# Kernel tuning notes

Hardware: AMD Instinct MI355X
Metric: run time of the kernel (lower is better)

## Reference

```python
import jax, jax.numpy as jnp
import numpy as np

N = 40000
E = 200000
D = 32
NUM_BANDS = 3
ORDER = 4
EPS = 1e-8
LN_EPS = 1e-5


def setup_inputs() -> dict:
    key = jax.random.key(0)
    ks = jax.random.split(key, 20)
    h = jax.random.normal(ks[0], (N, D), dtype=jnp.float32)
    Q = jax.random.normal(ks[1], (E, D, D), dtype=jnp.float32) / jnp.sqrt(jnp.float32(D))
    edge_index = jax.random.randint(ks[2], (2, E), 0, N, dtype=jnp.int32)
    coeffs = jnp.ones((NUM_BANDS, ORDER + 1), dtype=jnp.float32) / (ORDER + 1)
    s = 1.0 / np.sqrt(D)
    proj_W = jax.random.uniform(ks[3], (NUM_BANDS, D, D), minval=-s, maxval=s, dtype=jnp.float32)
    proj_b = jax.random.uniform(ks[4], (NUM_BANDS, D), minval=-s, maxval=s, dtype=jnp.float32)
    proj_g = jnp.ones((NUM_BANDS, D), dtype=jnp.float32)
    proj_beta = jnp.zeros((NUM_BANDS, D), dtype=jnp.float32)
    s3 = 1.0 / np.sqrt(NUM_BANDS * D)
    fus_W1 = jax.random.uniform(ks[5], (NUM_BANDS * D, D), minval=-s3, maxval=s3, dtype=jnp.float32)
    fus_b1 = jax.random.uniform(ks[6], (D,), minval=-s3, maxval=s3, dtype=jnp.float32)
    fus_g = jnp.ones((D,), dtype=jnp.float32)
    fus_beta = jnp.zeros((D,), dtype=jnp.float32)
    fus_W2 = jax.random.uniform(ks[7], (D, D), minval=-s, maxval=s, dtype=jnp.float32)
    fus_b2 = jax.random.uniform(ks[8], (D,), minval=-s, maxval=s, dtype=jnp.float32)
    return {"h": h, "Q": Q, "edge_index": edge_index, "coeffs": coeffs,
            "proj_W": proj_W, "proj_b": proj_b, "proj_g": proj_g, "proj_beta": proj_beta,
            "fus_W1": fus_W1, "fus_b1": fus_b1, "fus_g": fus_g, "fus_beta": fus_beta,
            "fus_W2": fus_W2, "fus_b2": fus_b2}


def _layer_norm(x, g, b):
    mu = x.mean(-1, keepdims=True)
    var = x.var(-1, keepdims=True)  # biased, as torch LayerNorm
    return (x - mu) / jnp.sqrt(var + LN_EPS) * g + b


def reference(h, Q, edge_index, coeffs, proj_W, proj_b, proj_g, proj_beta,
              fus_W1, fus_b1, fus_g, fus_beta, fus_W2, fus_b2):
    row, col = edge_index[0], edge_index[1]
    n = h.shape[0]
    ones_e = jnp.ones(row.shape[0], dtype=h.dtype)
    deg = (jax.ops.segment_sum(ones_e, row, num_segments=n)
           + jax.ops.segment_sum(ones_e, col, num_segments=n))  # [N]

    def matvec(x):
        # gather -> per-edge DxD bmm -> scatter_add; diag via degree
        Qh = jnp.einsum('eij,ej->ei', Q, x[col])          # [E, D]
        off = jax.ops.segment_sum(Qh, row, num_segments=n)  # [N, D]
        return deg[:, None] * x - off

    # power iteration for lambda_max (5 iters, fixed key for determinism)
    v = jax.random.normal(jax.random.key(42), h.shape, dtype=h.dtype)
    v = v / jnp.linalg.norm(v)
    lam = jnp.array(1.0, dtype=h.dtype)
    for _ in range(5):
        Lv = matvec(v)
        lam = (v * Lv).sum() / ((v * v).sum() + EPS)
        v = Lv / (jnp.linalg.norm(Lv) + EPS)
    lam = jnp.maximum(lam, 1.0)

    def L_tilde(x):
        return 2.0 / (lam + EPS) * matvec(x) - x

    bands = []
    for b_idx in range(NUM_BANDS):
        w = jax.nn.softmax(coeffs[b_idx])
        T_prev = h
        T_curr = L_tilde(h)
        res = w[0] * T_prev + w[1] * T_curr
        for k in range(2, ORDER + 1):
            T_next = 2.0 * L_tilde(T_curr) - T_prev
            res = res + w[k] * T_next
            T_prev, T_curr = T_curr, T_next
        p = jax.nn.silu(_layer_norm(res @ proj_W[b_idx] + proj_b[b_idx],
                                    proj_g[b_idx], proj_beta[b_idx]))
        bands.append(p)

    cat = jnp.concatenate(bands, axis=-1)  # [N, 3D]
    fused = jax.nn.silu(_layer_norm(cat @ fus_W1 + fus_b1, fus_g, fus_beta)) @ fus_W2 + fus_b2
    return h + fused
```

## Files before the change

kernel.cpp:

```cpp
#include <hip/hip_runtime.h>
#include <hip/hip_fp16.h>
#include <math.h>

#define NN 40000
#define EE 200000
#define DD 32
#define ND (NN * DD)
#define LNEPS 1e-5f

typedef float    fv4 __attribute__((ext_vector_type(4)));
typedef unsigned uv4 __attribute__((ext_vector_type(4)));

#define SLOT_ALPHA 48
#define SCAL_FLOATS (64 + 2048 + 64)

__device__ __forceinline__ void threefry2x32(unsigned k0, unsigned k1,
                                             unsigned x0, unsigned x1,
                                             unsigned& o0, unsigned& o1) {
  const unsigned k2 = k0 ^ k1 ^ 0x1BD11BDAu;
  unsigned v0 = x0 + k0, v1 = x1 + k1;
#define TF_ROUND(r) { v0 += v1; v1 = (v1 << (r)) | (v1 >> (32 - (r))); v1 ^= v0; }
  TF_ROUND(13) TF_ROUND(15) TF_ROUND(26) TF_ROUND(6)
  v0 += k1; v1 += k2 + 1u;
  TF_ROUND(17) TF_ROUND(29) TF_ROUND(16) TF_ROUND(24)
  v0 += k2; v1 += k0 + 2u;
  TF_ROUND(13) TF_ROUND(15) TF_ROUND(26) TF_ROUND(6)
  v0 += k0; v1 += k1 + 3u;
  TF_ROUND(17) TF_ROUND(29) TF_ROUND(16) TF_ROUND(24)
  v0 += k1; v1 += k2 + 4u;
  TF_ROUND(13) TF_ROUND(15) TF_ROUND(26) TF_ROUND(6)
  v0 += k2; v1 += k0 + 5u;
#undef TF_ROUND
  o0 = v0; o1 = v1;
}

__device__ __forceinline__ float wave64_sum(float x) {
  for (int o = 32; o > 0; o >>= 1) x += __shfl_xor(x, o, 64);
  return x;
}
__device__ __forceinline__ float g32_sum(float x) {
  for (int o = 16; o > 0; o >>= 1) x += __shfl_xor(x, o, 32);
  return x;
}

__global__ void k_deg(const int* __restrict__ ei, float* __restrict__ deg,
                      int* __restrict__ hist) {
  int e = blockIdx.x * 256 + threadIdx.x;
  if (e < EE) {
    int r = ei[e];
    atomicAdd(deg + r, 1.0f);
    atomicAdd(deg + ei[EE + e], 1.0f);
    atomicAdd(hist + r, 1);
  }
}

__global__ __launch_bounds__(1024) void k_scan(const int* __restrict__ hist,
                                               int* __restrict__ row_start,
                                               int* __restrict__ cursor) {
  __shared__ int part[1024];
  const int t = threadIdx.x;
  const int base = t * 40;
  int s = 0;
  for (int i = base; i < base + 40 && i < NN; ++i) s += hist[i];
  part[t] = s;
  __syncthreads();
  for (int off = 1; off < 1024; off <<= 1) {
    int v = (t >= off) ? part[t - off] : 0;
    __syncthreads();
    part[t] += v;
    __syncthreads();
  }
  int ex = (t == 0) ? 0 : part[t - 1];
  for (int i = base; i < base + 40 && i < NN; ++i) {
    row_start[i] = ex;
    cursor[i] = ex;
    ex += hist[i];
  }
  if (t == 0) row_start[NN] = EE;
}

__global__ void k_genv(float* __restrict__ v, float* __restrict__ vpre,
                       const float* __restrict__ deg) {
  int i = blockIdx.x * 256 + threadIdx.x;
  unsigned o0, o1;
  threefry2x32(0u, 42u, 0u, (unsigned)i, o0, o1);
  unsigned bits = o1;
  float f = __uint_as_float((bits >> 9) | 0x3f800000u) - 1.0f;
  const float lo = -0.99999994f;
  float u = fmaxf(lo, f * 2.0f + lo);
  float val = 1.41421354f * erfinvf(u);
  v[i] = val;
  if (vpre) vpre[i] = deg[i >> 5] * val;
}

__device__ __forceinline__ int clamp8(float q) {
  int v = (int)rintf(q);
  return v < -127 ? -127 : (v > 127 ? 127 : v);
}
__device__ __forceinline__ unsigned pack4v(fv4 q, float inv) {
  int q0 = clamp8(q.x * inv), q1 = clamp8(q.y * inv),
      q2 = clamp8(q.z * inv), q3 = clamp8(q.w * inv);
  return (q0 & 255) | ((q1 & 255) << 8) | ((q2 & 255) << 16) | ((q3 & 255) << 24);
}
__device__ __forceinline__ void dp4(unsigned u, fv4 xv, float& acc) {
  acc = fmaf((float)(signed char)(u),        xv.x, acc);
  acc = fmaf((float)(signed char)(u >> 8),   xv.y, acc);
  acc = fmaf((float)(signed char)(u >> 16),  xv.z, acc);
  acc = fmaf((float)(signed char)(u >> 24),  xv.w, acc);
}

__global__ __launch_bounds__(256) void k_cvt_mv(const float* __restrict__ x,
                                                const float* __restrict__ Q,
                                                const int* __restrict__ ei,
                                                int* __restrict__ cursor,
                                                char* __restrict__ Qi8,
                                                __half* __restrict__ Qs,
                                                int* __restrict__ cols,
                                                float* __restrict__ out) {
  const int slot = threadIdx.x >> 5;
  const int lane = threadIdx.x & 31;
  const int e = blockIdx.x * 8 + slot;
  const int row = ei[e];
  const int col = ei[EE + e];
  int pos = 0;
  if (lane == 0) pos = atomicAdd(cursor + row, 1);
  pos = __shfl(pos, 0, 32);
  const fv4* __restrict__ x4 = (const fv4*)(x + (size_t)col * DD);
  fv4 xr[8];
#pragma unroll
  for (int k = 0; k < 8; ++k) xr[k] = x4[k];
  const fv4* __restrict__ q4 =
      (const fv4*)(Q + (size_t)e * (DD * DD) + (size_t)lane * DD);
  fv4 qf[8];
#pragma unroll
  for (int k = 0; k < 8; ++k) qf[k] = __builtin_nontemporal_load(q4 + k);
  float acc = 0.0f;
#pragma unroll
  for (int k = 0; k < 8; ++k) {
    acc = fmaf(qf[k].x, xr[k].x, acc);
    acc = fmaf(qf[k].y, xr[k].y, acc);
    acc = fmaf(qf[k].z, xr[k].z, acc);
    acc = fmaf(qf[k].w, xr[k].w, acc);
  }
  float m = 0.0f;
#pragma unroll
  for (int k = 0; k < 8; ++k) {
    m = fmaxf(m, fmaxf(fmaxf(fabsf(qf[k].x), fabsf(qf[k].y)),
                       fmaxf(fabsf(qf[k].z), fabsf(qf[k].w))));
  }
  __half sh = __float2half(m * (1.0f / 127.0f));
  float s = __half2float(sh);
  float inv = (s > 0.0f) ? 1.0f / s : 0.0f;
  uv4 pa, pb;
  pa.x = pack4v(qf[0], inv); pa.y = pack4v(qf[1], inv);
  pa.z = pack4v(qf[2], inv); pa.w = pack4v(qf[3], inv);
  pb.x = pack4v(qf[4], inv); pb.y = pack4v(qf[5], inv);
  pb.z = pack4v(qf[6], inv); pb.w = pack4v(qf[7], inv);
  uv4* __restrict__ qs = (uv4*)(Qi8 + (size_t)pos * (DD * DD) + (size_t)lane * DD);
  qs[0] = pa;
  qs[1] = pb;
  Qs[pos * DD + lane] = sh;
  if (lane == 0) cols[pos] = col;
  atomicAdd(out + (size_t)row * DD + lane, -acc);
}

#define CHUNK 16

__global__ __launch_bounds__(256) void k_gather2(const float* __restrict__ px,
                                                 float* __restrict__ pout,
                                                 const float* __restrict__ kxv,
                                                 float* __restrict__ kout,
                                                 const char* __restrict__ Qi8,
                                                 const __half* __restrict__ Qs,
                                                 const int* __restrict__ cols,
                                                 const int* __restrict__ row_start,
                                                 const float* __restrict__ deg,
                                                 float* __restrict__ dots,
                                                 int do_dots) {
  __shared__ float lds[4][CHUNK][DD];
  __shared__ float d1[4], d2[4];
  const int NB = NN / 4;
  const bool isk = blockIdx.x >= NB;
  const int bid = isk ? blockIdx.x - NB : blockIdx.x;
  const float* __restrict__ x = isk ? kxv : px;
  float* __restrict__ out = isk ? kout : pout;

  const int wid  = threadIdx.x >> 6;
  const int lane = threadIdx.x & 63;
  const int half = lane >> 5;
  const int d    = lane & 31;
  const int r = bid * 4 + wid;
  const int beg = row_start[r];
  const int end = row_start[r + 1];
  const int degree = end - beg;

  const size_t idx = (size_t)r * DD + d;
  const float xi = x[idx];
  const float dv = deg[r];

  float acc = 0.0f;
  for (int chunk = 0; chunk < degree; chunk += CHUNK) {
    const int nchunk = min(CHUNK, degree - chunk);
    int myc = (lane < nchunk) ? cols[beg + chunk + lane] : 0;
    {
      const int el = lane >> 2;
      const int pt = lane & 3;
      if (el < nchunk) {
        const int c = __shfl(myc, el, 64);
        const fv4* __restrict__ xs = (const fv4*)(x + (size_t)c * DD);
        fv4 a = xs[pt * 2];
        fv4 b = xs[pt * 2 + 1];
        fv4* __restrict__ dst = (fv4*)&lds[wid][el][pt * 8];
        dst[0] = a;
        dst[1] = b;
      }
    }
    uv4 a0 = {0,0,0,0}, b0 = {0,0,0,0}, a1 = {0,0,0,0}, b1 = {0,0,0,0};
    float s0 = 0.0f, s1 = 0.0f;
#define LOADQ(PP, A, B, S)                                                    \
    if ((PP) < nchunk) {                                                      \
      const size_t pos = (size_t)(beg + chunk + (PP));                        \
      const uv4* __restrict__ q8 =                                            \
          (const uv4*)(Qi8 + pos * (DD * DD) + (size_t)d * DD);               \
      A = q8[0]; B = q8[1];                                                   \
      S = __half2float(Qs[pos * DD + d]);                                     \
    }
    LOADQ(half, a0, b0, s0)
    LOADQ(2 + half, a1, b1, s1)
    for (int p0 = 0; p0 < nchunk; p0 += 2) {
      uv4 a2 = {0,0,0,0}, b2 = {0,0,0,0};
      float s2 = 0.0f;
      LOADQ(p0 + 4 + half, a2, b2, s2)
      const int p = p0 + half;
      if (p < nchunk) {
        const fv4* __restrict__ xl = (const fv4*)&lds[wid][p][0];
        fv4 xr[8];
#pragma unroll
        for (int k = 0; k < 8; ++k) xr[k] = xl[k];
        float dot = 0.0f;
        dp4(a0.x, xr[0], dot); dp4(a0.y, xr[1], dot);
        dp4(a0.z, xr[2], dot); dp4(a0.w, xr[3], dot);
        dp4(b0.x, xr[4], dot); dp4(b0.y, xr[5], dot);
        dp4(b0.z, xr[6], dot); dp4(b0.w, xr[7], dot);
        acc = fmaf(s0, dot, acc);
      }
      a0 = a1; b0 = b1; s0 = s1;
      a1 = a2; b1 = b2; s1 = s2;
    }
#undef LOADQ
  }
  acc += __shfl_xor(acc, 32, 64);

  const float o = dv * xi - acc;
  if (half == 0) out[idx] = o;

  if (!isk && do_dots) {
    float p1 = (half == 0) ? o * xi : 0.0f;
    float p2 = (half == 0) ? xi * xi : 0.0f;
    p1 = wave64_sum(p1);
    p2 = wave64_sum(p2);
    if ((threadIdx.x & 63) == 0) { d1[wid] = p1; d2[wid] = p2; }
    __syncthreads();
    if (threadIdx.x == 0) {
      const int leaf = bid & 31;
      atomicAdd(dots + 64 + leaf * 32, d1[0] + d1[1] + d1[2] + d1[3]);
      atomicAdd(dots + 64 + 1024 + leaf * 32, d2[0] + d2[1] + d2[2] + d2[3]);
    }
  }
}

__global__ void k_pre(const float* __restrict__ x, const float* __restrict__ deg,
                      float* __restrict__ out) {
  int i = blockIdx.x * 256 + threadIdx.x;
  out[i] = deg[i >> 5] * x[i];
}

__global__ __launch_bounds__(256) void k_matvec(const float* __restrict__ x,
                                                const float* __restrict__ Q,
                                                const int* __restrict__ ei,
                                                float* __restrict__ out) {
  const int slot = threadIdx.x >> 5;
  const int lane = threadIdx.x & 31;
  const int e = blockIdx.x * 8 + slot;
  const int row = ei[e];
  const int col = ei[EE + e];
  const fv4* __restrict__ x4 = (const fv4*)(x + (size_t)col * DD);
  fv4 xr[8];
#pragma unroll
  for (int k = 0; k < 8; ++k) xr[k] = x4[k];
  const fv4* __restrict__ q4 =
      (const fv4*)(Q + (size_t)e * (DD * DD) + (size_t)lane * DD);
  float acc = 0.0f;
#pragma unroll
  for (int k = 0; k < 8; ++k) {
    fv4 q = q4[k];
    acc = fmaf(q.x, xr[k].x, acc);
    acc = fmaf(q.y, xr[k].y, acc);
    acc = fmaf(q.z, xr[k].z, acc);
    acc = fmaf(q.w, xr[k].w, acc);
  }
  atomicAdd(out + (size_t)row * DD + lane, -acc);
}

#define DOT_BLOCKS 640
__global__ void k_dots(const float* __restrict__ u4, const float* __restrict__ u5,
                       float* __restrict__ scal) {
  float s1 = 0.0f, s2 = 0.0f;
  for (int i = blockIdx.x * 256 + threadIdx.x; i < ND; i += DOT_BLOCKS * 256) {
    float a = u4[i], b = u5[i];
    s1 = fmaf(a, b, s1);
    s2 = fmaf(a, a, s2);
  }
  s1 = wave64_sum(s1);
  s2 = wave64_sum(s2);
  __shared__ float ls1[4], ls2[4];
  int w = threadIdx.x >> 6;
  if ((threadIdx.x & 63) == 0) { ls1[w] = s1; ls2[w] = s2; }
  __syncthreads();
  if (threadIdx.x == 0) {
    atomicAdd(scal + 64, ls1[0] + ls1[1] + ls1[2] + ls1[3]);
    atomicAdd(scal + 64 + 1024, ls2[0] + ls2[1] + ls2[2] + ls2[3]);
  }
}

__global__ void k_alpha(float* __restrict__ scal) {
  float S1 = 0.0f, S2 = 0.0f;
  for (int l = 0; l < 32; ++l) {
    S1 += scal[64 + l * 32];
    S2 += scal[64 + 1024 + l * 32];
  }
  float lam = S1 / S2 / (1.0f + 1e-8f);
  lam = fmaxf(lam, 1.0f);
  scal[SLOT_ALPHA] = 2.0f / (lam + 1e-8f);
}

__global__ __launch_bounds__(256) void k_fuse(
    const float* __restrict__ h,
    const float* __restrict__ W1, const float* __restrict__ W2,
    const float* __restrict__ W3, const float* __restrict__ W4,
    const float* __restrict__ scal,
    const float* __restrict__ coeffs,
    const float* __restrict__ projW, const float* __restrict__ projb,
    const float* __restrict__ projg, const float* __restrict__ projbeta,
    const float* __restrict__ fusW1, const float* __restrict__ fusb1,
    const float* __restrict__ fusg, const float* __restrict__ fusbeta,
    const float* __restrict__ fusW2, const float* __restrict__ fusb2,
    float* __restrict__ out) {
  __shared__ float s_res[8][3][DD];
  __shared__ float s_p[8][3 * DD];
  __shared__ float s_s[8][DD];
  const int slot = threadIdx.x >> 5;
  const int lane = threadIdx.x & 31;
  const int n = blockIdx.x * 8 + slot;

  float w[3][5];
#pragma unroll
  for (int b = 0; b < 3; ++b) {
    float m = -1e30f;
#pragma unroll
    for (int k = 0; k < 5; ++k) m = fmaxf(m, coeffs[b * 5 + k]);
    float s = 0.0f;
#pragma unroll
    for (int k = 0; k < 5; ++k) { w[b][k] = expf(coeffs[b * 5 + k] - m); s += w[b][k]; }
#pragma unroll
    for (int k = 0; k < 5; ++k) w[b][k] /= s;
  }

  const float C[5][5] = {
      { 1.0f,   0.0f,   0.0f,   0.0f,  0.0f},
      {-1.0f,   1.0f,   0.0f,   0.0f,  0.0f},
      { 1.0f,  -4.0f,   2.0f,   0.0f,  0.0f},
      {-1.0f,   9.0f, -12.0f,   4.0f,  0.0f},
      { 1.0f, -16.0f,  40.0f, -32.0f,  8.0f}};
  float cb[3][5];
#pragma unroll
  for (int b = 0; b < 3; ++b)
#pragma unroll
    for (int j = 0; j < 5; ++j) {
      float c = 0.0f;
#pragma unroll
      for (int k = 0; k < 5; ++k) c = fmaf(w[b][k], C[k][j], c);
      cb[b][j] = c;
    }

  const float alpha = scal[SLOT_ALPHA];
  const float a1 = alpha, a2 = a1 * alpha, a3 = a2 * alpha, a4 = a3 * alpha;

  const int idx = n * DD + lane;
  const float hd = h[idx];
  float y[5];
  y[0] = hd;
  y[1] = a1 * W1[idx];
  y[2] = a2 * W2[idx];
  y[3] = a3 * W3[idx];
  y[4] = a4 * W4[idx];
#pragma unroll
  for (int b = 0; b < 3; ++b) {
    float res = 0.0f;
#pragma unroll
    for (int j = 0; j < 5; ++j) res = fmaf(cb[b][j], y[j], res);
    s_res[slot][b][lane] = res;
  }
  __syncthreads();

#pragma unroll
  for (int b = 0; b < 3; ++b) {
    float yv = projb[b * DD + lane];
#pragma unroll
    for (int j = 0; j < DD; ++j)
      yv = fmaf(s_res[slot][b][j], projW[(b * DD + j) * DD + lane], yv);
    float mu = g32_sum(yv) * (1.0f / DD);
    float dv = yv - mu;
    float var = g32_sum(dv * dv) * (1.0f / DD);
    float z = dv * rsqrtf(var + LNEPS) * projg[b * DD + lane] + projbeta[b * DD + lane];
    float pb = z / (1.0f + expf(-z));
    s_p[slot][b * DD + lane] = pb;
  }
  __syncthreads();

  float yv = fusb1[lane];
#pragma unroll
  for (int j = 0; j < 3 * DD; ++j)
    yv = fmaf(s_p[slot][j], fusW1[j * DD + lane], yv);
  float mu = g32_sum(yv) * (1.0f / DD);
  float dv = yv - mu;
  float var = g32_sum(dv * dv) * (1.0f / DD);
  float z = dv * rsqrtf(var + LNEPS) * fusg[lane] + fusbeta[lane];
  float sv = z / (1.0f + expf(-z));
  s_s[slot][lane] = sv;
  __syncthreads();

  float o = fusb2[lane];
#pragma unroll
  for (int j = 0; j < DD; ++j)
    o = fmaf(s_s[slot][j], fusW2[j * DD + lane], o);
  out[idx] = hd + o;
}

extern "C" void kernel_launch(void* const* d_in, const int* in_sizes, int n_in,
                              void* d_out, int out_size, void* d_ws, size_t ws_size,
                              hipStream_t stream) {
  (void)in_sizes; (void)n_in; (void)out_size;
  const float* h        = (const float*)d_in[0];
  const float* Q        = (const float*)d_in[1];
  const int*   ei       = (const int*)d_in[2];
  const float* coeffs   = (const float*)d_in[3];
  const float* projW    = (const float*)d_in[4];
  const float* projb    = (const float*)d_in[5];
  const float* projg    = (const float*)d_in[6];
  const float* projbeta = (const float*)d_in[7];
  const float* fusW1    = (const float*)d_in[8];
  const float* fusb1    = (const float*)d_in[9];
  const float* fusg     = (const float*)d_in[10];
  const float* fusbeta  = (const float*)d_in[11];
  const float* fusW2    = (const float*)d_in[12];
  const float* fusb2    = (const float*)d_in[13];
  float* out = (float*)d_out;

  const size_t qi_bytes  = (size_t)EE * DD * DD;
  const size_t qs_bytes  = (size_t)EE * DD * sizeof(__half);
  const size_t col_bytes = (size_t)EE * sizeof(int);
  const size_t idx_bytes = (size_t)(2 * NN + 2) * sizeof(int);
  const size_t f32_elems = 6u * (size_t)ND + 2u * NN + SCAL_FLOATS;
  const size_t meta = qi_bytes + qs_bytes + col_bytes + idx_bytes;
  const size_t need = meta + f32_elems * sizeof(float) + 512;
  const bool fast = ws_size >= need;

  char*   Qi8 = (char*)d_ws;
  __half* Qs  = (__half*)((char*)d_ws + qi_bytes);
  int*  cols      = (int*)((char*)d_ws + qi_bytes + qs_bytes);
  int*  row_start = cols + EE;
  int*  cursor    = row_start + NN + 1;
  float* base = fast
      ? (float*)((char*)d_ws + ((meta + 255) & ~(size_t)255))
      : (float*)d_ws;
  float* uA   = base;
  float* uB   = uA + ND;
  float* W1   = uB + ND;
  float* W2   = W1 + ND;
  float* W3   = W2 + ND;
  float* W4   = W3 + ND;
  float* deg  = W4 + ND;
  float* scal = deg + NN;
  int*   hist = (int*)(scal + SCAL_FLOATS);

  (void)hipMemsetAsync(deg, 0, (2 * (size_t)NN + SCAL_FLOATS) * sizeof(float),
                       stream);

  k_deg<<<(EE + 255) / 256, 256, 0, stream>>>(ei, deg, hist);

  if (fast) {
    k_genv<<<ND / 256, 256, 0, stream>>>(uA, uB, deg);
    k_scan<<<1, 1024, 0, stream>>>(hist, row_start, cursor);
    k_cvt_mv<<<EE / 8, 256, 0, stream>>>(uA, Q, ei, cursor, Qi8, Qs, cols, uB);

    const int G2 = 2 * (NN / 4);
    k_gather2<<<G2, 256, 0, stream>>>(uB, uA, h,  W1, Qi8, Qs, cols,
                                      row_start, deg, scal, 0);
    k_gather2<<<G2, 256, 0, stream>>>(uA, uB, W1, W2, Qi8, Qs, cols,
                                      row_start, deg, scal, 0);
    k_gather2<<<G2, 256, 0, stream>>>(uB, uA, W2, W3, Qi8, Qs, cols,
                                      row_start, deg, scal, 0);
    k_gather2<<<G2, 256, 0, stream>>>(uA, uB, W3, W4, Qi8, Qs, cols,
                                      row_start, deg, scal, 1);
    k_alpha<<<1, 1, 0, stream>>>(scal);
  } else {
    k_genv<<<ND / 256, 256, 0, stream>>>(uA, nullptr, deg);
    float* cur = uA;
    float* nxt = uB;
    for (int it = 0; it < 5; ++it) {
      k_pre<<<ND / 256, 256, 0, stream>>>(cur, deg, nxt);
      k_matvec<<<EE / 8, 256, 0, stream>>>(cur, Q, ei, nxt);
      float* t = cur; cur = nxt; nxt = t;
    }
    k_dots<<<DOT_BLOCKS, 256, 0, stream>>>(nxt, cur, scal);
    k_alpha<<<1, 1, 0, stream>>>(scal);
    const float* xin[4] = {h, W1, W2, W3};
    float* wout[4]      = {W1, W2, W3, W4};
    for (int k = 0; k < 4; ++k) {
      k_pre<<<ND / 256, 256, 0, stream>>>(xin[k], deg, wout[k]);
      k_matvec<<<EE / 8, 256, 0, stream>>>(xin[k], Q, ei, wout[k]);
    }
  }

  k_fuse<<<NN / 8, 256, 0, stream>>>(h, W1, W2, W3, W4, scal, coeffs,
                                     projW, projb, projg, projbeta,
                                     fusW1, fusb1, fusg, fusbeta,
                                     fusW2, fusb2, out);
}
```

Measured before the change: 911.8 us.

## Process two rows per wave in gather kernel and fold alpha into fuse

Each wave in the CSR gather kernel now handles two rows (r and r+N/2) at once, interleaving their Q loads and LDS neighbour tiles so more independent memory requests are in flight per wave, and the grid is halved. The Q prefetch distance drops from two pairs ahead to one. The single-thread k_alpha kernel is removed and every k_fuse thread recomputes lambda/alpha from the 32 partial sums, saving a launch at the cost of redundant scalar reads. The two-row scheme adds imbalance when the two rows' degrees differ and raises register and LDS use.

Result: no change. 920.0 us (+0.9%).

```diff
diff --git a/kernel.cpp b/kernel.cpp
--- a/kernel.cpp
+++ b/kernel.cpp
@@ -177,9 +177,9 @@
                                                  const float* __restrict__ deg,
                                                  float* __restrict__ dots,
                                                  int do_dots) {
-  __shared__ float lds[4][CHUNK][DD];
+  __shared__ float lds[4][2][CHUNK][DD];
   __shared__ float d1[4], d2[4];
-  const int NB = NN / 4;
+  const int NB = NN / 8;
   const bool isk = blockIdx.x >= NB;
   const int bid = isk ? blockIdx.x - NB : blockIdx.x;
   const float* __restrict__ x = isk ? kxv : px;
@@ -189,74 +189,112 @@
   const int lane = threadIdx.x & 63;
   const int half = lane >> 5;
   const int d    = lane & 31;
-  const int r = bid * 4 + wid;
-  const int beg = row_start[r];
-  const int end = row_start[r + 1];
-  const int degree = end - beg;
-
-  const size_t idx = (size_t)r * DD + d;
-  const float xi = x[idx];
-  const float dv = deg[r];
-
-  float acc = 0.0f;
-  for (int chunk = 0; chunk < degree; chunk += CHUNK) {
-    const int nchunk = min(CHUNK, degree - chunk);
-    int myc = (lane < nchunk) ? cols[beg + chunk + lane] : 0;
+  const int rA = bid * 4 + wid;
+  const int rB = rA + NN / 2;
+  const int begA = row_start[rA];
+  const int endA = row_start[rA + 1];
+  const int begB = row_start[rB];
+  const int endB = row_start[rB + 1];
+  const int degA = endA - begA;
+  const int degB = endB - begB;
+  const int degmax = max(degA, degB);
+
+  const size_t idxA = (size_t)rA * DD + d;
+  const size_t idxB = (size_t)rB * DD + d;
+  const float xiA = x[idxA];
+  const float xiB = x[idxB];
+  const float dvA = deg[rA];
+  const float dvB = deg[rB];
+
+  float accA = 0.0f, accB = 0.0f;
+  for (int chunk = 0; chunk < degmax; chunk += CHUNK) {
+    const int nA = min(CHUNK, max(0, degA - chunk));
+    const int nB = min(CHUNK, max(0, degB - chunk));
+    int mycA = (lane < nA) ? cols[begA + chunk + lane] : 0;
+    int mycB = (lane < nB) ? cols[begB + chunk + lane] : 0;
     {
       const int el = lane >> 2;
       const int pt = lane & 3;
-      if (el < nchunk) {
-        const int c = __shfl(myc, el, 64);
+      if (el < nA) {
+        const int c = __shfl(mycA, el, 64);
         const fv4* __restrict__ xs = (const fv4*)(x + (size_t)c * DD);
         fv4 a = xs[pt * 2];
         fv4 b = xs[pt * 2 + 1];
-        fv4* __restrict__ dst = (fv4*)&lds[wid][el][pt * 8];
+        fv4* __restrict__ dst = (fv4*)&lds[wid][0][el][pt * 8];
         dst[0] = a;
         dst[1] = b;
       }
-    }
-    uv4 a0 = {0,0,0,0}, b0 = {0,0,0,0}, a1 = {0,0,0,0}, b1 = {0,0,0,0};
-    float s0 = 0.0f, s1 = 0.0f;
-#define LOADQ(PP, A, B, S)                                                    \
-    if ((PP) < nchunk) {                                                      \
-      const size_t pos = (size_t)(beg + chunk + (PP));                        \
+      if (el < nB) {
+        const int c = __shfl(mycB, el, 64);
+        const fv4* __restrict__ xs = (const fv4*)(x + (size_t)c * DD);
+        fv4 a = xs[pt * 2];
+        fv4 b = xs[pt * 2 + 1];
+        fv4* __restrict__ dst = (fv4*)&lds[wid][1][el][pt * 8];
+        dst[0] = a;
+        dst[1] = b;
+      }
+    }
+    uv4 aA = {0,0,0,0}, bA = {0,0,0,0}, aB = {0,0,0,0}, bB = {0,0,0,0};
+    float sA = 0.0f, sB = 0.0f;
+#define LOADQ(BEG, PP, NC, A, B, S)                                           \
+    if ((PP) < (NC)) {                                                        \
+      const size_t pos = (size_t)((BEG) + chunk + (PP));                      \
       const uv4* __restrict__ q8 =                                            \
           (const uv4*)(Qi8 + pos * (DD * DD) + (size_t)d * DD);               \
       A = q8[0]; B = q8[1];                                                   \
       S = __half2float(Qs[pos * DD + d]);                                     \
     }
-    LOADQ(half, a0, b0, s0)
-    LOADQ(2 + half, a1, b1, s1)
-    for (int p0 = 0; p0 < nchunk; p0 += 2) {
-      uv4 a2 = {0,0,0,0}, b2 = {0,0,0,0};
-      float s2 = 0.0f;
-      LOADQ(p0 + 4 + half, a2, b2, s2)
+    LOADQ(begA, half, nA, aA, bA, sA)
+    LOADQ(begB, half, nB, aB, bB, sB)
+    const int nmax = max(nA, nB);
+    for (int p0 = 0; p0 < nmax; p0 += 2) {
+      uv4 aA2 = {0,0,0,0}, bA2 = {0,0,0,0}, aB2 = {0,0,0,0}, bB2 = {0,0,0,0};
+      float sA2 = 0.0f, sB2 = 0.0f;
+      LOADQ(begA, p0 + 2 + half, nA, aA2, bA2, sA2)
+      LOADQ(begB, p0 + 2 + half, nB, aB2, bB2, sB2)
       const int p = p0 + half;
-      if (p < nchunk) {
-        const fv4* __restrict__ xl = (const fv4*)&lds[wid][p][0];
+      if (p < nA) {
+        const fv4* __restrict__ xl = (const fv4*)&lds[wid][0][p][0];
         fv4 xr[8];
 #pragma unroll
         for (int k = 0; k < 8; ++k) xr[k] = xl[k];
         float dot = 0.0f;
-        dp4(a0.x, xr[0], dot); dp4(a0.y, xr[1], dot);
-        dp4(a0.z, xr[2], dot); dp4(a0.w, xr[3], dot);
-        dp4(b0.x, xr[4], dot); dp4(b0.y, xr[5], dot);
-        dp4(b0.z, xr[6], dot); dp4(b0.w, xr[7], dot);
-        acc = fmaf(s0, dot, acc);
+        dp4(aA.x, xr[0], dot); dp4(aA.y, xr[1], dot);
+        dp4(aA.z, xr[2], dot); dp4(aA.w, xr[3], dot);
+        dp4(bA.x, xr[4], dot); dp4(bA.y, xr[5], dot);
+        dp4(bA.z, xr[6], dot); dp4(bA.w, xr[7], dot);
+        accA = fmaf(sA, dot, accA);
       }
-      a0 = a1; b0 = b1; s0 = s1;
-      a1 = a2; b1 = b2; s1 = s2;
+      if (p < nB) {
+        const fv4* __restrict__ xl = (const fv4*)&lds[wid][1][p][0];
+        fv4 xr[8];
+#pragma unroll
+        for (int k = 0; k < 8; ++k) xr[k] = xl[k];
+        float dot = 0.0f;
+        dp4(aB.x, xr[0], dot); dp4(aB.y, xr[1], dot);
+        dp4(aB.z, xr[2], dot); dp4(aB.w, xr[3], dot);
+        dp4(bB.x, xr[4], dot); dp4(bB.y, xr[5], dot);
+        dp4(bB.z, xr[6], dot); dp4(bB.w, xr[7], dot);
+        accB = fmaf(sB, dot, accB);
+      }
+      aA = aA2; bA = bA2; sA = sA2;
+      aB = aB2; bB = bB2; sB = sB2;
     }
 #undef LOADQ
   }
-  acc += __shfl_xor(acc, 32, 64);
-
-  const float o = dv * xi - acc;
-  if (half == 0) out[idx] = o;
+  accA += __shfl_xor(accA, 32, 64);
+  accB += __shfl_xor(accB, 32, 64);
+
+  const float oA = dvA * xiA - accA;
+  const float oB = dvB * xiB - accB;
+  if (half == 0) {
+    out[idxA] = oA;
+    out[idxB] = oB;
+  }
 
   if (!isk && do_dots) {
-    float p1 = (half == 0) ? o * xi : 0.0f;
-    float p2 = (half == 0) ? xi * xi : 0.0f;
+    float p1 = (half == 0) ? oA * xiA + oB * xiB : 0.0f;
+    float p2 = (half == 0) ? xiA * xiA + xiB * xiB : 0.0f;
     p1 = wave64_sum(p1);
     p2 = wave64_sum(p2);
     if ((threadIdx.x & 63) == 0) { d1[wid] = p1; d2[wid] = p2; }
@@ -321,17 +359,6 @@
     atomicAdd(scal + 64, ls1[0] + ls1[1] + ls1[2] + ls1[3]);
     atomicAdd(scal + 64 + 1024, ls2[0] + ls2[1] + ls2[2] + ls2[3]);
   }
-}
-
-__global__ void k_alpha(float* __restrict__ scal) {
-  float S1 = 0.0f, S2 = 0.0f;
-  for (int l = 0; l < 32; ++l) {
-    S1 += scal[64 + l * 32];
-    S2 += scal[64 + 1024 + l * 32];
-  }
-  float lam = S1 / S2 / (1.0f + 1e-8f);
-  lam = fmaxf(lam, 1.0f);
-  scal[SLOT_ALPHA] = 2.0f / (lam + 1e-8f);
 }
 
 __global__ __launch_bounds__(256) void k_fuse(
@@ -353,6 +380,16 @@
   const int lane = threadIdx.x & 31;
   const int n = blockIdx.x * 8 + slot;
 
+  float S1 = 0.0f, S2 = 0.0f;
+#pragma unroll
+  for (int l = 0; l < 32; ++l) {
+    S1 += scal[64 + l * 32];
+    S2 += scal[64 + 1024 + l * 32];
+  }
+  float lam = S1 / S2 / (1.0f + 1e-8f);
+  lam = fmaxf(lam, 1.0f);
+  const float alpha = 2.0f / (lam + 1e-8f);
+
   float w[3][5];
 #pragma unroll
   for (int b = 0; b < 3; ++b) {
@@ -383,7 +420,6 @@
       cb[b][j] = c;
     }
 
-  const float alpha = scal[SLOT_ALPHA];
   const float a1 = alpha, a2 = a1 * alpha, a3 = a2 * alpha, a4 = a3 * alpha;
 
   const int idx = n * DD + lane;
@@ -494,7 +530,7 @@
     k_scan<<<1, 1024, 0, stream>>>(hist, row_start, cursor);
     k_cvt_mv<<<EE / 8, 256, 0, stream>>>(uA, Q, ei, cursor, Qi8, Qs, cols, uB);
 
-    const int G2 = 2 * (NN / 4);
+    const int G2 = 2 * (NN / 8);
     k_gather2<<<G2, 256, 0, stream>>>(uB, uA, h,  W1, Qi8, Qs, cols,
                                       row_start, deg, scal, 0);
     k_gather2<<<G2, 256, 0, stream>>>(uA, uB, W1, W2, Qi8, Qs, cols,
@@ -503,7 +539,6 @@
                                       row_start, deg, scal, 0);
     k_gather2<<<G2, 256, 0, stream>>>(uA, uB, W3, W4, Qi8, Qs, cols,
                                       row_start, deg, scal, 1);
-    k_alpha<<<1, 1, 0, stream>>>(scal);
   } else {
     k_genv<<<ND / 256, 256, 0, stream>>>(uA, nullptr, deg);
     float* cur = uA;
@@ -514,7 +549,6 @@
       float* t = cur; cur = nxt; nxt = t;
     }
     k_dots<<<DOT_BLOCKS, 256, 0, stream>>>(nxt, cur, scal);
-    k_alpha<<<1, 1, 0, stream>>>(scal);
     const float* xin[4] = {h, W1, W2, W3};
     float* wout[4]      = {W1, W2, W3, W4};
     for (int k = 0; k < 4; ++k) {
```
